# Kernel optimization log

Measured on AMD Instinct MI355X. Metric: run time of the kernel, lower is better.

The kernel has to match this reference:

```python
import jax, jax.numpy as jnp
import numpy as np
import math

B, N, F, H = 16, 256, 1024, 16
HD = F // H  # head_dim = 64
NEG = -9e15


def setup_inputs() -> dict:
    key = jax.random.key(0)
    ks = jax.random.split(key, 12)
    s = 0.02
    return {
        "obj_feats": jax.random.normal(ks[0], (B, N, F), jnp.float32),
        "cross_feats": jax.random.normal(ks[1], (B, N, F), jnp.float32),
        "adj_matrix": jax.random.randint(ks[2], (B, N, N), 0, 2, jnp.int32),
        "label_biases_att": jax.random.normal(ks[3], (B, N, N), jnp.float32),
        "Wq": jax.random.normal(ks[4], (F, F), jnp.float32) * s,
        "bq": jnp.zeros((F,), jnp.float32),
        "Wk": jax.random.normal(ks[5], (F, F), jnp.float32) * s,
        "bk": jnp.zeros((F,), jnp.float32),
        "Wv": jax.random.normal(ks[6], (F, F), jnp.float32) * s,
        "bv": jnp.zeros((F,), jnp.float32),
        # grouped 1x1 conv: out=F, groups=H, in_per_group=F -> weight [F, F]
        "Wo": jax.random.normal(ks[7], (F, F), jnp.float32) * s,
        "bo": jnp.zeros((F,), jnp.float32),
    }


def reference(obj_feats, cross_feats, adj_matrix, label_biases_att,
              Wq, bq, Wk, bk, Wv, bv, Wo, bo):
    # projections (torch Linear: x @ W.T + b)
    q = (jnp.einsum('bnf,gf->bng', obj_feats, Wq) + bq).reshape(B, N, H, HD)
    k = (jnp.einsum('bnf,gf->bng', cross_feats, Wk) + bk).reshape(B, N, H, HD)
    v = jnp.einsum('bnf,gf->bng', cross_feats, Wv) + bv          # [B, N, F] (NOT split per head)

    scale = 1.0 / math.sqrt(float(HD))
    att = jnp.einsum('bqhd,bkhd->bqhk', q, k) * scale            # [B, Nq, H, Nk]

    # adjacency mask broadcast over heads + label bias (both indexed [b, q, k])
    mask = (adj_matrix > 0)[:, :, None, :]                       # [B, Nq, 1, Nk]
    att = jnp.where(mask, att, NEG) + label_biases_att[:, :, None, :]

    p = jax.nn.softmax(att, axis=-1)                             # softmax over keys

    # weighted sum against un-split values: [B, Nq, H, Nk] x [B, Nk, F]
    out = jnp.einsum('bqhk,bkf->bqhf', p, v)                     # [B, Nq, H, F]

    # grouped 1x1 conv: group h maps its F input channels -> HD output channels
    Wo_g = Wo.reshape(H, HD, F)
    out = jnp.einsum('bqhf,hdf->bqhd', out, Wo_g) + bo.reshape(H, HD)
    out = out.reshape(B, N, F)

    att_mean = p.sum(axis=2) / H                                 # [B, Nq, Nk]
    return out, att_mean
```

## Files before the change

### kernel.cpp

```cpp
#include <hip/hip_runtime.h>

#define NEGF -9e15f

typedef __attribute__((ext_vector_type(8))) unsigned short u16x8;
typedef __attribute__((ext_vector_type(8))) short          s16x8;
typedef __attribute__((ext_vector_type(4))) float          f32x4;

__device__ __forceinline__ unsigned short f2bf(float x) {
  union { float f; unsigned int u; } c; c.f = x;
  unsigned int r = c.u + 0x7fffu + ((c.u >> 16) & 1u);
  return (unsigned short)(r >> 16);
}
__device__ __forceinline__ float bf2f(unsigned short v) {
  union { float f; unsigned int u; } c; c.u = ((unsigned int)v) << 16;
  return c.f;
}

__device__ __forceinline__ void gload16(const void* g, void* l) {
  __builtin_amdgcn_global_load_lds(
      (const __attribute__((address_space(1))) unsigned int*)g,
      (__attribute__((address_space(3))) unsigned int*)l, 16, 0, 0);
}

__global__ __launch_bounds__(256) void cvt2_bf16(
    const float* __restrict__ a, const float* __restrict__ b,
    unsigned short* __restrict__ oa, unsigned short* __restrict__ ob)
{
  const int bid = blockIdx.x;
  const float* in = (bid < 4096) ? a : b;
  unsigned short* out = (bid < 4096) ? oa : ob;
  const int i = ((bid & 4095) * 256 + threadIdx.x) * 4;
  const float4 v = *(const float4*)(in + i);
  ushort4 o;
  o.x = f2bf(v.x); o.y = f2bf(v.y); o.z = f2bf(v.z); o.w = f2bf(v.w);
  *(ushort4*)(out + i) = o;
}

__global__ __launch_bounds__(256) void prep_w(
    const float* __restrict__ Wq, const float* __restrict__ Wk,
    const float* __restrict__ Wo, const float* __restrict__ Wv,
    unsigned short* __restrict__ Wall, unsigned short* __restrict__ Wo_bf,
    unsigned short* __restrict__ Wvt_bf)
{
  __shared__ float tile[32][33];
  const int bid = blockIdx.x;
  if (bid < 3072) {
    const int i = ((bid & 1023) * 256 + threadIdx.x) * 4;
    const float* in;
    unsigned short* out;
    float sc = 1.f;
    if (bid < 1024)      { in = Wq; out = Wall;           sc = 0.125f; }
    else if (bid < 2048) { in = Wk; out = Wall + 1048576; }
    else                 { in = Wo; out = Wo_bf; }
    const float4 v = *(const float4*)(in + i);
    ushort4 o;
    o.x = f2bf(v.x * sc); o.y = f2bf(v.y * sc);
    o.z = f2bf(v.z * sc); o.w = f2bf(v.w * sc);
    *(ushort4*)(out + i) = o;
  } else {
    const int j = bid - 3072;
    const int bc = (j & 31) * 32, br = (j >> 5) * 32;
    const int tx = threadIdx.x & 31, ty8 = threadIdx.x >> 5;
    #pragma unroll
    for (int jj = 0; jj < 32; jj += 8)
      tile[ty8 + jj][tx] = Wv[(size_t)(br + ty8 + jj) * 1024 + bc + tx];
    __syncthreads();
    #pragma unroll
    for (int jj = 0; jj < 32; jj += 8)
      Wvt_bf[(size_t)(bc + ty8 + jj) * 1024 + br + tx] = f2bf(tile[tx][ty8 + jj]);
  }
}

__global__ __launch_bounds__(256) void prep_bias(
    const float* __restrict__ bq, const float* __restrict__ bk,
    const float* __restrict__ Wo, const float* __restrict__ bv,
    float* __restrict__ ball)
{
  const int bid = blockIdx.x;
  if (bid < 4) {
    const int i = bid * 256 + threadIdx.x;
    ball[i]        = 0.125f * bq[i];
    ball[1024 + i] = bk[i];
  } else {
    const int g    = (bid - 4) * 4 + (threadIdx.x >> 6);
    const int lane = threadIdx.x & 63;
    float acc = 0.f;
    for (int f = lane; f < 1024; f += 64)
      acc = fmaf(Wo[(size_t)g * 1024 + f], bv[f], acc);
    #pragma unroll
    for (int off = 32; off > 0; off >>= 1) acc += __shfl_down(acc, off);
    if (lane == 0) ball[2048 + g] = acc;
  }
}

__global__ __launch_bounds__(256) void mb_prep(
    const int* __restrict__ adj, const float* __restrict__ lab,
    float* __restrict__ mb)
{
  const int i = (blockIdx.x * 256 + threadIdx.x) * 4;
  const int4   a = *(const int4*)(adj + i);
  const float4 l = *(const float4*)(lab + i);
  float4 o;
  o.x = a.x > 0 ? l.x : NEGF;
  o.y = a.y > 0 ? l.y : NEGF;
  o.z = a.z > 0 ? l.z : NEGF;
  o.w = a.w > 0 ? l.w : NEGF;
  *(float4*)(mb + i) = o;
}

__global__ __launch_bounds__(256, 3) void gemm_wov(
    const unsigned short* __restrict__ A,
    const unsigned short* __restrict__ Bw,
    unsigned short* __restrict__ Cout)
{
  __shared__ unsigned short Asm[128 * 64];
  __shared__ unsigned short Bsm[64 * 64];
  const int t = threadIdx.x;
  const int lane = t & 63, w = t >> 6;
  const int wm = w >> 1, wn = w & 1;
  const int bm = blockIdx.y * 128, bn = blockIdx.x * 64;

  const int srow = lane >> 3;
  const int skel = (lane & 7) * 8;
  const int fr = lane & 15, kf = (lane >> 4) * 8;

  f32x4 acc[4][2] = {};

  for (int k0 = 0; k0 < 1024; k0 += 64) {
    if (k0) __syncthreads();
    #pragma unroll
    for (int i = 0; i < 4; ++i) {
      const int c = i * 4 + w;
      const int r = c * 8 + srow;
      gload16(A + (size_t)(bm + r) * 1024 + k0 + skel, &Asm[c * 512]);
    }
    #pragma unroll
    for (int i = 0; i < 2; ++i) {
      const int c = i * 4 + w;
      const int r = c * 8 + srow;
      gload16(Bw + (size_t)(bn + r) * 1024 + k0 + skel, &Bsm[c * 512]);
    }
    __syncthreads();
    #pragma unroll
    for (int kk = 0; kk < 2; ++kk) {
      s16x8 af[4], bf[2];
      #pragma unroll
      for (int fm = 0; fm < 4; ++fm)
        af[fm] = *(const s16x8*)&Asm[(wm * 64 + fm * 16 + fr) * 64 + kk * 32 + kf];
      #pragma unroll
      for (int fn = 0; fn < 2; ++fn)
        bf[fn] = *(const s16x8*)&Bsm[(wn * 32 + fn * 16 + fr) * 64 + kk * 32 + kf];
      #pragma unroll
      for (int fm = 0; fm < 4; ++fm)
        #pragma unroll
        for (int fn = 0; fn < 2; ++fn)
          acc[fm][fn] = __builtin_amdgcn_mfma_f32_16x16x32_bf16(af[fm], bf[fn], acc[fm][fn], 0, 0, 0);
    }
  }

  const int rg = (lane >> 4) * 4;
  #pragma unroll
  for (int fm = 0; fm < 4; ++fm)
    #pragma unroll
    for (int fn = 0; fn < 2; ++fn) {
      const int col = bn + wn * 32 + fn * 16 + fr;
      #pragma unroll
      for (int r = 0; r < 4; ++r) {
        const int row = bm + wm * 64 + fm * 16 + rg + r;
        Cout[(size_t)row * 1024 + col] = f2bf(acc[fm][fn][r]);
      }
    }
}

__global__ __launch_bounds__(512, 2) void gemm_big(
    const unsigned short* __restrict__ objA,
    const unsigned short* __restrict__ crossA,
    const unsigned short* __restrict__ Wall,
    const float* __restrict__ ball,
    unsigned short* __restrict__ Qo,
    unsigned short* __restrict__ Ko,
    unsigned short* __restrict__ VWt)
{
  __shared__ __align__(16) char smem[131072];
  const int t = threadIdx.x;
  const int wid = t >> 6, lane = t & 63;
  const int wm = wid >> 2, wn = wid & 3;
  const int fr = lane & 15, grp = lane >> 4;

  const int bid = blockIdx.x;
  const int xcd = bid & 7, j = bid >> 3;
  const int bmi = (xcd >> 1) * 4 + j / 6;
  const int bni = (xcd & 1) * 6 + j % 6;
  const int bm = bmi * 256, bn = bni * 256;
  const unsigned short* Ag = ((bni < 4) ? objA : crossA) + (size_t)bm * 1024;
  const unsigned short* Bg = Wall + (size_t)bn * 1024;

  const int r8 = lane >> 3, cb = (lane & 7) * 16;

  f32x4 acc[8][4] = {};
  s16x8 bfr[4][2];
  s16x8 aq[2][2];

  auto CH = [&](int buf, int isB, int q, int k0) {
    const int row = q * 64 + wid * 8 + r8;
    const int sc  = cb ^ ((row & 7) << 4);
    const unsigned short* src = isB ? Bg : Ag;
    gload16((const char*)(src + (size_t)row * 1024 + k0) + sc,
            smem + buf * 65536 + isB * 32768 + q * 8192 + wid * 1024);
  };

#define BAR() { asm volatile("" ::: "memory"); __builtin_amdgcn_s_barrier(); asm volatile("" ::: "memory"); }
#define RDB(BUF)                                                             \
  { _Pragma("unroll") for (int fn = 0; fn < 4; ++fn)                         \
      _Pragma("unroll") for (int kk = 0; kk < 2; ++kk) {                     \
        const int row = wn * 64 + fn * 16 + fr;                              \
        bfr[fn][kk] = *(const s16x8*)((BUF) + 32768 + row * 128 +            \
            ((kk * 64 + grp * 16) ^ ((row & 7) << 4)));                      \
      } }
#define RDA(BUF, P)                                                          \
  { _Pragma("unroll") for (int fm = 0; fm < 2; ++fm)                         \
      _Pragma("unroll") for (int kk = 0; kk < 2; ++kk) {                     \
        const int row = wm * 128 + (2 * (P) + fm) * 16 + fr;                 \
        aq[fm][kk] = *(const s16x8*)((BUF) + row * 128 +                     \
            ((kk * 64 + grp * 16) ^ ((row & 7) << 4)));                      \
      } }
#define MMQ(P)                                                               \
  { __builtin_amdgcn_s_setprio(1);                                           \
    _Pragma("unroll") for (int fm = 0; fm < 2; ++fm)                         \
      _Pragma("unroll") for (int fn = 0; fn < 4; ++fn) {                     \
        acc[2 * (P) + fm][fn] = __builtin_amdgcn_mfma_f32_16x16x32_bf16(     \
            aq[fm][0], bfr[fn][0], acc[2 * (P) + fm][fn], 0, 0, 0);          \
        acc[2 * (P) + fm][fn] = __builtin_amdgcn_mfma_f32_16x16x32_bf16(     \
            aq[fm][1], bfr[fn][1], acc[2 * (P) + fm][fn], 0, 0, 0);          \
      }                                                                      \
    __builtin_amdgcn_s_setprio(0); }
#define TILE4(BUF)                                                           \
  RDB(BUF); RDA(BUF, 0); BAR(); MMQ(0); BAR();                               \
  RDA(BUF, 1); BAR(); MMQ(1); BAR();                                         \
  RDA(BUF, 2); BAR(); MMQ(2); BAR();                                         \
  RDA(BUF, 3); BAR(); MMQ(3); BAR();

  CH(0, 1, 0, 0); CH(0, 1, 1, 0); CH(0, 1, 2, 0); CH(0, 1, 3, 0);
  CH(0, 0, 0, 0); CH(0, 0, 1, 0); CH(0, 0, 2, 0); CH(0, 0, 3, 0);
  CH(1, 1, 0, 64); CH(1, 1, 1, 64); CH(1, 1, 2, 64); CH(1, 1, 3, 64);
  CH(1, 0, 0, 64); CH(1, 0, 2, 64);

  #pragma unroll 2
  for (int kt = 0; kt < 14; ++kt) {
    const int cur = kt & 1;
    char* bufc = smem + cur * 65536;
    const int k1 = (kt + 1) * 64, k2 = (kt + 2) * 64;
    CH(cur ^ 1, 0, 1, k1);
    CH(cur ^ 1, 0, 3, k1);
    asm volatile("s_waitcnt vmcnt(8)" ::: "memory");
    BAR();
    RDB(bufc); RDA(bufc, 0);
    BAR(); MMQ(0); BAR();
    RDA(bufc, 1); CH(cur, 1, 0, k2); CH(cur, 1, 1, k2);
    BAR(); MMQ(1); BAR();
    RDA(bufc, 2); CH(cur, 1, 2, k2); CH(cur, 1, 3, k2);
    BAR(); MMQ(2); BAR();
    RDA(bufc, 3); CH(cur, 0, 0, k2); CH(cur, 0, 2, k2);
    BAR(); MMQ(3); BAR();
  }
  CH(1, 0, 1, 960); CH(1, 0, 3, 960);
  asm volatile("s_waitcnt vmcnt(8)" ::: "memory");
  BAR();
  TILE4(smem);
  asm volatile("s_waitcnt vmcnt(0)" ::: "memory");
  BAR();
  TILE4(smem + 65536);

#undef BAR
#undef RDB
#undef RDA
#undef MMQ
#undef TILE4

  const int rg = grp * 4;
  const int mode = bn >> 10;
  #pragma unroll
  for (int fm = 0; fm < 8; ++fm) {
    #pragma unroll
    for (int fn = 0; fn < 4; ++fn) {
      const int col  = bn + wn * 64 + fn * 16 + fr;
      const int cl   = col & 1023;
      const float bb = ball[col];
      const int row0 = bm + wm * 128 + fm * 16 + rg;
      if (mode == 0) {
        #pragma unroll
        for (int r = 0; r < 4; ++r)
          Qo[(size_t)(row0 + r) * 1024 + cl] = f2bf(acc[fm][fn][r] + bb);
      } else if (mode == 1) {
        #pragma unroll
        for (int r = 0; r < 4; ++r)
          Ko[(size_t)(row0 + r) * 1024 + cl] = f2bf(acc[fm][fn][r] + bb);
      } else {
        const int bidx = row0 >> 8, tok = row0 & 255;
        ushort4 u;
        u.x = f2bf(acc[fm][fn][0] + bb);
        u.y = f2bf(acc[fm][fn][1] + bb);
        u.z = f2bf(acc[fm][fn][2] + bb);
        u.w = f2bf(acc[fm][fn][3] + bb);
        *(ushort4*)(VWt + ((size_t)bidx * 1024 + cl) * 256 + tok) = u;
      }
    }
  }
}

__global__ __launch_bounds__(256, 2) void attn_mfma(
    const unsigned short* __restrict__ Qg,
    const unsigned short* __restrict__ Kg,
    const unsigned short* __restrict__ VWt,
    const float* __restrict__ mb,
    const float* __restrict__ bo,
    float* __restrict__ outp, unsigned short* __restrict__ Pb)
{
  const int t = threadIdx.x;
  const int w = t >> 6, lane = t & 63;
  const int fr = lane & 15, grp = lane >> 4;
  const int bid = blockIdx.x;
  const int xcd = bid & 7, i = bid >> 3;
  const int h   = i & 15;
  const int bqt = xcd * 8 + (i >> 4);
  const int b   = bqt >> 2;
  const int qt  = bqt & 3;
  const int q0 = qt * 64 + w * 16;

  __shared__ __align__(16) unsigned short Ks[256 * 64];
  __shared__ __align__(16) unsigned short VWs[64 * 256];

  {
    const unsigned short* kb = Kg + (size_t)(b * 256) * 1024 + h * 64;
    const int colb = (lane & 7) * 16;
    #pragma unroll
    for (int c = 0; c < 8; ++c) {
      const int row = c * 32 + w * 8 + (lane >> 3);
      const int sb  = colb ^ ((row & 7) << 4);
      gload16(kb + (size_t)row * 1024 + (sb >> 1), (char*)Ks + c * 4096 + w * 1024);
    }
  }
  {
    const unsigned short* vwb = VWt + (size_t)(b * 16 + h) * 16384;
    const int xb = (lane & 31) * 16;
    #pragma unroll
    for (int c = 0; c < 8; ++c) {
      const int row = c * 8 + w * 2 + (lane >> 5);
      const int sb  = xb ^ ((row & 7) << 4);
      gload16(vwb + row * 256 + (sb >> 1), (char*)VWs + c * 4096 + w * 1024);
    }
  }

  const unsigned short* qp = Qg + ((size_t)(b * 256 + q0 + fr)) * 1024 + h * 64 + grp * 8;
  const s16x8 qf0 = *(const s16x8*)qp;
  const s16x8 qf1 = *(const s16x8*)(qp + 32);

  __syncthreads();

  const float* mbp = mb + ((size_t)(b * 256 + q0 + fr)) * 256 + grp * 4;
  const int colA = (grp * 16) ^ ((fr & 7) << 4);

  f32x4 s[16];
  #pragma unroll
  for (int nf = 0; nf < 16; ++nf) s[nf] = (f32x4){0.f, 0.f, 0.f, 0.f};

  s16x8 kA[8], kB[8];
  float4 mA[4], mB[4];
  float mx = -3e38f;

#define LOADB(KF, MF, nb)                                                    \
  { _Pragma("unroll") for (int i2 = 0; i2 < 4; ++i2) {                       \
      const char* rp = (const char*)Ks + (((nb)*4 + i2) * 16 + fr) * 128;    \
      KF[2*i2]   = *(const s16x8*)(rp + colA);                               \
      KF[2*i2+1] = *(const s16x8*)(rp + (colA ^ 64));                        \
      MF[i2]     = *(const float4*)(mbp + ((nb)*4 + i2) * 16); } }
#define MFMAB(KF, nb)                                                        \
  { _Pragma("unroll") for (int i2 = 0; i2 < 4; ++i2) {                       \
      s[(nb)*4+i2] = __builtin_amdgcn_mfma_f32_16x16x32_bf16(KF[2*i2],   qf0, s[(nb)*4+i2], 0, 0, 0); \
      s[(nb)*4+i2] = __builtin_amdgcn_mfma_f32_16x16x32_bf16(KF[2*i2+1], qf1, s[(nb)*4+i2], 0, 0, 0); } }
#define MASKB(MF, nb)                                                        \
  { _Pragma("unroll") for (int i2 = 0; i2 < 4; ++i2) {                       \
      _Pragma("unroll") for (int r = 0; r < 4; ++r) {                        \
        const float m = ((const float*)&MF[i2])[r];                          \
        const float v = (m > -1e14f) ? s[(nb)*4+i2][r] + m : m;              \
        s[(nb)*4+i2][r] = v; mx = fmaxf(mx, v); } } }

  LOADB(kA, mA, 0); LOADB(kB, mB, 1); MFMAB(kA, 0);
  MASKB(mA, 0);     LOADB(kA, mA, 2); MFMAB(kB, 1);
  MASKB(mB, 1);     LOADB(kB, mB, 3); MFMAB(kA, 2);
  MASKB(mA, 2);     LOADB(kA, mA, 4); MFMAB(kB, 3);
  MASKB(mB, 3);     LOADB(kB, mB, 5); MFMAB(kA, 4);
  MASKB(mA, 4);     LOADB(kA, mA, 6); MFMAB(kB, 5);
  MASKB(mB, 5);     LOADB(kB, mB, 7); MFMAB(kA, 6);
  MASKB(mA, 6);     MFMAB(kB, 7);     MASKB(mB, 7);
#undef LOADB
#undef MFMAB
#undef MASKB

  mx = fmaxf(mx, __shfl_xor(mx, 16));
  mx = fmaxf(mx, __shfl_xor(mx, 32));
  float sm = 0.f;
  #pragma unroll
  for (int nf = 0; nf < 16; ++nf)
    #pragma unroll
    for (int r = 0; r < 4; ++r) {
      const float e = __expf(s[nf][r] - mx);
      s[nf][r] = e;
      sm += e;
    }
  sm += __shfl_xor(sm, 16);
  sm += __shfl_xor(sm, 32);
  const float inv = 1.f / sm;

  uint2 u2[16];
  #pragma unroll
  for (int nf = 0; nf < 16; ++nf) {
    const unsigned lo = (unsigned)f2bf(s[nf][0] * inv) | ((unsigned)f2bf(s[nf][1] * inv) << 16);
    const unsigned hi = (unsigned)f2bf(s[nf][2] * inv) | ((unsigned)f2bf(s[nf][3] * inv) << 16);
    u2[nf] = make_uint2(lo, hi);
  }

  unsigned short* prow = Pb + (((size_t)(b * 16 + h)) * 256 + q0 + fr) * 256 + grp * 4;
  #pragma unroll
  for (int nf = 0; nf < 16; ++nf)
    *(uint2*)(prow + nf * 16) = u2[nf];

  f32x4 o[4];
  #pragma unroll
  for (int nf = 0; nf < 4; ++nf) o[nf] = (f32x4){0.f, 0.f, 0.f, 0.f};
  const int srcA = fr + ((grp & 1) << 5);
  const int srcB = srcA + 16;
  const int swz  = (fr & 7) << 4;
  const bool hiSel = (grp & 2);
  #pragma unroll
  for (int ks = 0; ks < 8; ++ks) {
    const int aLx = __shfl((int)u2[2 * ks].x,     srcA, 64);
    const int aLy = __shfl((int)u2[2 * ks].y,     srcA, 64);
    const int bLx = __shfl((int)u2[2 * ks].x,     srcB, 64);
    const int bLy = __shfl((int)u2[2 * ks].y,     srcB, 64);
    const int aHx = __shfl((int)u2[2 * ks + 1].x, srcA, 64);
    const int aHy = __shfl((int)u2[2 * ks + 1].y, srcA, 64);
    const int bHx = __shfl((int)u2[2 * ks + 1].x, srcB, 64);
    const int bHy = __shfl((int)u2[2 * ks + 1].y, srcB, 64);
    union { int4 i; s16x8 v; } pf;
    pf.i = hiSel ? make_int4(aHx, aHy, bHx, bHy) : make_int4(aLx, aLy, bLx, bLy);
    const int cbv = (ks * 64 + grp * 16) ^ swz;
    #pragma unroll
    for (int nf = 0; nf < 4; ++nf) {
      const s16x8 vf = *(const s16x8*)((const char*)VWs + (nf * 16 + fr) * 512 + cbv);
      o[nf] = __builtin_amdgcn_mfma_f32_16x16x32_bf16(pf.v, vf, o[nf], 0, 0, 0);
    }
  }

  #pragma unroll
  for (int nf = 0; nf < 4; ++nf) {
    const float bb = bo[h * 64 + nf * 16 + fr];
    #pragma unroll
    for (int r = 0; r < 4; ++r)
      outp[((size_t)b * 256 + q0 + grp * 4 + r) * 1024 + h * 64 + nf * 16 + fr]
          = o[nf][r] + bb;
  }
}

__global__ __launch_bounds__(256) void attm_reduce(
    const unsigned short* __restrict__ Pb, float* __restrict__ attm)
{
  const size_t idx = (size_t)blockIdx.x * 256 + threadIdx.x;
  const int    k8  = (int)(idx & 31);
  const size_t bq  = idx >> 5;
  const int    b   = (int)(bq >> 8);
  const int    q   = (int)(bq & 255);
  float s[8] = {};
  const unsigned short* base = Pb + (size_t)b * 1048576 + (size_t)q * 256 + k8 * 8;
  #pragma unroll
  for (int hh = 0; hh < 16; ++hh) {
    const u16x8 p = *(const u16x8*)(base + (size_t)hh * 65536);
    #pragma unroll
    for (int j = 0; j < 8; ++j) s[j] += bf2f(p[j]);
  }
  float* dst = attm + bq * 256 + k8 * 8;
  float4 r0, r1;
  r0.x = s[0] * 0.0625f; r0.y = s[1] * 0.0625f; r0.z = s[2] * 0.0625f; r0.w = s[3] * 0.0625f;
  r1.x = s[4] * 0.0625f; r1.y = s[5] * 0.0625f; r1.z = s[6] * 0.0625f; r1.w = s[7] * 0.0625f;
  *(float4*)dst = r0;
  *(float4*)(dst + 4) = r1;
}

extern "C" void kernel_launch(void* const* d_in, const int* in_sizes, int n_in,
                              void* d_out, int out_size, void* d_ws, size_t ws_size,
                              hipStream_t stream)
{
  const float* obj   = (const float*)d_in[0];
  const float* cross = (const float*)d_in[1];
  const int*   adj   = (const int*)d_in[2];
  const float* lab   = (const float*)d_in[3];
  const float* Wq    = (const float*)d_in[4];
  const float* bq    = (const float*)d_in[5];
  const float* Wk    = (const float*)d_in[6];
  const float* bk    = (const float*)d_in[7];
  const float* Wv    = (const float*)d_in[8];
  const float* bv    = (const float*)d_in[9];
  const float* Wo    = (const float*)d_in[10];
  const float* bo    = (const float*)d_in[11];

  float* out  = (float*)d_out;
  float* attm = out + (size_t)16 * 256 * 1024;

  char* ws = (char*)d_ws;
  unsigned short* obj_bf   = (unsigned short*)(ws + 0);
  unsigned short* cross_bf = (unsigned short*)(ws + 8388608);
  unsigned short* Qbf      = (unsigned short*)(ws + 16777216);
  unsigned short* Kbf      = (unsigned short*)(ws + 25165824);
  unsigned short* VWt      = (unsigned short*)(ws + 33554432);
  unsigned short* Wall     = (unsigned short*)(ws + 41943040);
  unsigned short* Wo_bf    = (unsigned short*)(ws + 48234496);
  unsigned short* Wvt_bf   = (unsigned short*)(ws + 50331648);
  float*          ball     = (float*)(ws + 50331648);
  unsigned short* Pbuf     = (unsigned short*)(ws + 52432896);
  float*          mbuf     = (float*)obj_bf;

  cvt2_bf16<<<8192, 256, 0, stream>>>(obj, cross, obj_bf, cross_bf);
  prep_w<<<4096, 256, 0, stream>>>(Wq, Wk, Wo, Wv, Wall, Wo_bf, Wvt_bf);

  gemm_wov<<<dim3(16, 8), 256, 0, stream>>>(Wo_bf, Wvt_bf, Wall + 2097152);

  prep_bias<<<260, 256, 0, stream>>>(bq, bk, Wo, bv, ball);

  gemm_big<<<192, 512, 0, stream>>>(
      obj_bf, cross_bf, Wall, ball, Qbf, Kbf, VWt);

  mb_prep<<<1024, 256, 0, stream>>>(adj, lab, mbuf);

  attn_mfma<<<1024, 256, 0, stream>>>(
      Qbf, Kbf, VWt, mbuf, bo, out, Pbuf);
  attm_reduce<<<512, 256, 0, stream>>>(Pbuf, attm);
}
```

Before: 118.1 us.

## Fuse prep kernels into one launch and double attention block to 128 queries

Merges the input conversion, weight conversion/transpose, bias prep and mask prep kernels into a single prep_all launch when the workspace is large enough, giving the mask its own buffer so it no longer aliases obj_bf. The attention kernel now uses 512-thread blocks covering 128 queries per (batch, head), so each K/VW tile staged in LDS is shared by twice as many query rows and half as many blocks launch. This cuts launch count and redundant K/V loads, at the cost of a larger, more heterogeneous prep grid and possibly lower occupancy in attention.

```diff
diff --git a/kernel.cpp b/kernel.cpp
--- a/kernel.cpp
+++ b/kernel.cpp
@@ -106,6 +106,82 @@
   o.z = a.z > 0 ? l.z : NEGF;
   o.w = a.w > 0 ? l.w : NEGF;
   *(float4*)(mb + i) = o;
+}
+
+__global__ __launch_bounds__(256) void prep_all(
+    const float* __restrict__ obj, const float* __restrict__ cross,
+    const float* __restrict__ Wq, const float* __restrict__ Wk,
+    const float* __restrict__ Wo, const float* __restrict__ Wv,
+    const float* __restrict__ bq, const float* __restrict__ bk,
+    const float* __restrict__ bv,
+    const int* __restrict__ adj, const float* __restrict__ lab,
+    unsigned short* __restrict__ obj_bf, unsigned short* __restrict__ cross_bf,
+    unsigned short* __restrict__ Wall, unsigned short* __restrict__ Wo_bf,
+    unsigned short* __restrict__ Wvt_bf,
+    float* __restrict__ ball, float* __restrict__ mb)
+{
+  __shared__ float tile[32][33];
+  const int bid = blockIdx.x;
+  if (bid < 8192) {
+    const float* in = (bid < 4096) ? obj : cross;
+    unsigned short* out = (bid < 4096) ? obj_bf : cross_bf;
+    const int i = ((bid & 4095) * 256 + threadIdx.x) * 4;
+    const float4 v = *(const float4*)(in + i);
+    ushort4 o;
+    o.x = f2bf(v.x); o.y = f2bf(v.y); o.z = f2bf(v.z); o.w = f2bf(v.w);
+    *(ushort4*)(out + i) = o;
+  } else if (bid < 11264) {
+    const int wb = bid - 8192;
+    const int i = ((wb & 1023) * 256 + threadIdx.x) * 4;
+    const float* in;
+    unsigned short* out;
+    float sc = 1.f;
+    if (wb < 1024)      { in = Wq; out = Wall;           sc = 0.125f; }
+    else if (wb < 2048) { in = Wk; out = Wall + 1048576; }
+    else                { in = Wo; out = Wo_bf; }
+    const float4 v = *(const float4*)(in + i);
+    ushort4 o;
+    o.x = f2bf(v.x * sc); o.y = f2bf(v.y * sc);
+    o.z = f2bf(v.z * sc); o.w = f2bf(v.w * sc);
+    *(ushort4*)(out + i) = o;
+  } else if (bid < 12288) {
+    const int j = bid - 11264;
+    const int bc = (j & 31) * 32, br = (j >> 5) * 32;
+    const int tx = threadIdx.x & 31, ty8 = threadIdx.x >> 5;
+    #pragma unroll
+    for (int jj = 0; jj < 32; jj += 8)
+      tile[ty8 + jj][tx] = Wv[(size_t)(br + ty8 + jj) * 1024 + bc + tx];
+    __syncthreads();
+    #pragma unroll
+    for (int jj = 0; jj < 32; jj += 8)
+      Wvt_bf[(size_t)(bc + ty8 + jj) * 1024 + br + tx] = f2bf(tile[tx][ty8 + jj]);
+  } else if (bid < 12548) {
+    const int pb = bid - 12288;
+    if (pb < 4) {
+      const int i = pb * 256 + threadIdx.x;
+      ball[i]        = 0.125f * bq[i];
+      ball[1024 + i] = bk[i];
+    } else {
+      const int g    = (pb - 4) * 4 + (threadIdx.x >> 6);
+      const int lane = threadIdx.x & 63;
+      float acc = 0.f;
+      for (int f = lane; f < 1024; f += 64)
+        acc = fmaf(Wo[(size_t)g * 1024 + f], bv[f], acc);
+      #pragma unroll
+      for (int off = 32; off > 0; off >>= 1) acc += __shfl_down(acc, off);
+      if (lane == 0) ball[2048 + g] = acc;
+    }
+  } else {
+    const int i = ((bid - 12548) * 256 + threadIdx.x) * 4;
+    const int4   a = *(const int4*)(adj + i);
+    const float4 l = *(const float4*)(lab + i);
+    float4 o;
+    o.x = a.x > 0 ? l.x : NEGF;
+    o.y = a.y > 0 ? l.y : NEGF;
+    o.z = a.z > 0 ? l.z : NEGF;
+    o.w = a.w > 0 ? l.w : NEGF;
+    *(float4*)(mb + i) = o;
+  }
 }
 
 __global__ __launch_bounds__(256, 3) void gemm_wov(
@@ -308,7 +384,7 @@
   }
 }
 
-__global__ __launch_bounds__(256, 2) void attn_mfma(
+__global__ __launch_bounds__(512, 4) void attn_mfma(
     const unsigned short* __restrict__ Qg,
     const unsigned short* __restrict__ Kg,
     const unsigned short* __restrict__ VWt,
@@ -317,15 +393,15 @@
     float* __restrict__ outp, unsigned short* __restrict__ Pb)
 {
   const int t = threadIdx.x;
-  const int w = t >> 6, lane = t & 63;
+  const int wid = t >> 6, lane = t & 63;
   const int fr = lane & 15, grp = lane >> 4;
   const int bid = blockIdx.x;
   const int xcd = bid & 7, i = bid >> 3;
-  const int h   = i & 15;
-  const int bqt = xcd * 8 + (i >> 4);
-  const int b   = bqt >> 2;
-  const int qt  = bqt & 3;
-  const int q0 = qt * 64 + w * 16;
+  const int h    = i & 15;
+  const int r2   = i >> 4;
+  const int half = r2 & 1;
+  const int b    = xcd * 2 + (r2 >> 1);
+  const int q0 = half * 128 + wid * 16;
 
   __shared__ __align__(16) unsigned short Ks[256 * 64];
   __shared__ __align__(16) unsigned short VWs[64 * 256];
@@ -334,20 +410,20 @@
     const unsigned short* kb = Kg + (size_t)(b * 256) * 1024 + h * 64;
     const int colb = (lane & 7) * 16;
     #pragma unroll
-    for (int c = 0; c < 8; ++c) {
-      const int row = c * 32 + w * 8 + (lane >> 3);
+    for (int c = 0; c < 4; ++c) {
+      const int row = c * 64 + wid * 8 + (lane >> 3);
       const int sb  = colb ^ ((row & 7) << 4);
-      gload16(kb + (size_t)row * 1024 + (sb >> 1), (char*)Ks + c * 4096 + w * 1024);
+      gload16(kb + (size_t)row * 1024 + (sb >> 1), (char*)Ks + c * 8192 + wid * 1024);
     }
   }
   {
     const unsigned short* vwb = VWt + (size_t)(b * 16 + h) * 16384;
     const int xb = (lane & 31) * 16;
     #pragma unroll
-    for (int c = 0; c < 8; ++c) {
-      const int row = c * 8 + w * 2 + (lane >> 5);
+    for (int c = 0; c < 4; ++c) {
+      const int row = c * 16 + wid * 2 + (lane >> 5);
       const int sb  = xb ^ ((row & 7) << 4);
-      gload16(vwb + row * 256 + (sb >> 1), (char*)VWs + c * 4096 + w * 1024);
+      gload16(vwb + row * 256 + (sb >> 1), (char*)VWs + c * 8192 + wid * 1024);
     }
   }
 
@@ -515,23 +591,30 @@
   unsigned short* Wall     = (unsigned short*)(ws + 41943040);
   unsigned short* Wo_bf    = (unsigned short*)(ws + 48234496);
   unsigned short* Wvt_bf   = (unsigned short*)(ws + 50331648);
-  float*          ball     = (float*)(ws + 50331648);
   unsigned short* Pbuf     = (unsigned short*)(ws + 52432896);
-  float*          mbuf     = (float*)obj_bf;
-
-  cvt2_bf16<<<8192, 256, 0, stream>>>(obj, cross, obj_bf, cross_bf);
-  prep_w<<<4096, 256, 0, stream>>>(Wq, Wk, Wo, Wv, Wall, Wo_bf, Wvt_bf);
-
-  gemm_wov<<<dim3(16, 8), 256, 0, stream>>>(Wo_bf, Wvt_bf, Wall + 2097152);
-
-  prep_bias<<<260, 256, 0, stream>>>(bq, bk, Wo, bv, ball);
-
-  gemm_big<<<192, 512, 0, stream>>>(
-      obj_bf, cross_bf, Wall, ball, Qbf, Kbf, VWt);
-
-  mb_prep<<<1024, 256, 0, stream>>>(adj, lab, mbuf);
-
-  attn_mfma<<<1024, 256, 0, stream>>>(
-      Qbf, Kbf, VWt, mbuf, bo, out, Pbuf);
-  attm_reduce<<<512, 256, 0, stream>>>(Pbuf, attm);
-}
+
+  const bool big_ws = ws_size >= (size_t)104857600;
+
+  if (big_ws) {
+    float* ball = (float*)(ws + 92274688);
+    float* mbuf = (float*)(ws + 96468992);
+    prep_all<<<13572, 256, 0, stream>>>(
+        obj, cross, Wq, Wk, Wo, Wv, bq, bk, bv, adj, lab,
+        obj_bf, cross_bf, Wall, Wo_bf, Wvt_bf, ball, mbuf);
+    gemm_wov<<<dim3(16, 8), 256, 0, stream>>>(Wo_bf, Wvt_bf, Wall + 2097152);
+    gemm_big<<<192, 512, 0, stream>>>(obj_bf, cross_bf, Wall, ball, Qbf, Kbf, VWt);
+    attn_mfma<<<512, 512, 0, stream>>>(Qbf, Kbf, VWt, mbuf, bo, out, Pbuf);
+    attm_reduce<<<512, 256, 0, stream>>>(Pbuf, attm);
+  } else {
+    float* ball = (float*)(ws + 50331648);
+    float* mbuf = (float*)obj_bf;
+    cvt2_bf16<<<8192, 256, 0, stream>>>(obj, cross, obj_bf, cross_bf);
+    prep_w<<<4096, 256, 0, stream>>>(Wq, Wk, Wo, Wv, Wall, Wo_bf, Wvt_bf);
+    gemm_wov<<<dim3(16, 8), 256, 0, stream>>>(Wo_bf, Wvt_bf, Wall + 2097152);
+    prep_bias<<<260, 256, 0, stream>>>(bq, bk, Wo, bv, ball);
+    gemm_big<<<192, 512, 0, stream>>>(obj_bf, cross_bf, Wall, ball, Qbf, Kbf, VWt);
+    mb_prep<<<1024, 256, 0, stream>>>(adj, lab, mbuf);
+    attn_mfma<<<512, 512, 0, stream>>>(Qbf, Kbf, VWt, mbuf, bo, out, Pbuf);
+    attm_reduce<<<512, 256, 0, stream>>>(Pbuf, attm);
+  }
+}
```

Measured after the change: 111.3 us. 5.8% less time.
